# Optimization experiments

Hardware: AMD Instinct MI355X
Metric: run time of the kernel (lower is better)

## Reference

```python
import jax, jax.numpy as jnp
import numpy as np

N = 8192
IN_C = 256
OUT_C = 64
ALPHA = 0.2  # LeakyReLU negative slope
NEG_INF = -9e15


def setup_inputs() -> dict:
    key = jax.random.key(0)
    k1, k2, k3, k4 = jax.random.split(key, 4)
    x = jax.random.normal(k1, (N, IN_C), dtype=jnp.float32)
    adjacent = jax.random.randint(k2, (N, N), 0, 2, dtype=jnp.int32)
    # xavier_uniform with gain=1.2: limit = gain * sqrt(6/(fan_in+fan_out))
    lim_w = 1.2 * np.sqrt(6.0 / (IN_C + OUT_C))
    w = jax.random.uniform(k3, (IN_C, OUT_C), dtype=jnp.float32, minval=-lim_w, maxval=lim_w)
    lim_a = 1.2 * np.sqrt(6.0 / (2 * OUT_C + 1))
    a = jax.random.uniform(k4, (2 * OUT_C, 1), dtype=jnp.float32, minval=-lim_a, maxval=lim_a)
    return {"x": x, "adjacent": adjacent, "w": w, "a": a}


def reference(x, adjacent, w, a):
    # h: [N, out]
    h = x @ w
    # e_ij = LeakyReLU(a^T [h_i || h_j]) computed without materializing [N,N,2*out]:
    # split a into source/target halves -> rank-1 broadcast sum.
    a_src = a[:OUT_C, 0]   # [out]
    a_dst = a[OUT_C:, 0]   # [out]
    f_src = h @ a_src      # [N]
    f_dst = h @ a_dst      # [N]
    e = f_src[:, None] + f_dst[None, :]            # [N, N]
    e = jnp.where(e > 0, e, ALPHA * e)             # LeakyReLU
    # mask by adjacency, softmax over neighbors (rows)
    e = jnp.where(adjacent > 0, e, NEG_INF)
    attention = jax.nn.softmax(e, axis=-1)         # [N, N]
    h_prime = attention @ h                        # [N, out]
    # concat=True -> ELU activation
    return jax.nn.elu(h_prime)
```

## Files before the change

### kernel.cpp

```cpp
#include <hip/hip_runtime.h>
#include <hip/hip_bf16.h>

#define N 8192
#define IN_C 256
#define OUT_C 64
#define ALPHA 0.2f
#define L2E 1.44269504f

typedef short bf16x8 __attribute__((ext_vector_type(8)));
typedef float f32x4 __attribute__((ext_vector_type(4)));

#define OFF_H      0u
#define OFF_HT     2097152u
#define OFF_FS     3145728u
#define OFF_FD     3178496u
#define OFF_FDMAX  3211264u
#define OFF_NUM    3211520u

__global__ __launch_bounds__(256) void k_linear(const float* __restrict__ x,
                                                const float* __restrict__ w,
                                                const float* __restrict__ a,
                                                float* __restrict__ h,
                                                float* __restrict__ fs,
                                                float* __restrict__ fd) {
    __shared__ float wl[IN_C * OUT_C];
    int t = threadIdx.x;
    for (int idx = t; idx < IN_C * OUT_C; idx += 256) wl[idx] = w[idx];
    __syncthreads();
    int i = blockIdx.x * 4 + (t >> 6);
    int c = t & 63;
    const float* xr = x + (size_t)i * IN_C;
    float acc = 0.f;
#pragma unroll 8
    for (int k = 0; k < IN_C; ++k) acc = fmaf(xr[k], wl[k * 64 + c], acc);
    h[(size_t)i * 64 + c] = acc;
    float s = acc * a[c];
    float d = acc * a[64 + c];
#pragma unroll
    for (int off = 32; off > 0; off >>= 1) {
        s += __shfl_xor(s, off, 64);
        d += __shfl_xor(d, off, 64);
    }
    if (c == 0) { fs[i] = s; fd[i] = d; }
}

__global__ __launch_bounds__(256) void k_tr(const float* __restrict__ h,
                                            __hip_bfloat16* __restrict__ ht) {
    __shared__ __hip_bfloat16 lds[64 * 65];
    int t = threadIdx.x;
    int i0 = blockIdx.x * 64;
#pragma unroll
    for (int k = 0; k < 16; ++k) {
        int idx = k * 256 + t;
        int il = idx >> 6, c = idx & 63;
        lds[c * 65 + il] = __float2bfloat16(h[(size_t)(i0 + il) * 64 + c]);
    }
    __syncthreads();
#pragma unroll
    for (int k = 0; k < 16; ++k) {
        int idx = k * 256 + t;
        int c = idx >> 6, il = idx & 63;
        ht[(size_t)c * N + i0 + il] = lds[c * 65 + il];
    }
}

__global__ __launch_bounds__(256) void k_fdmax(const float* __restrict__ fd,
                                               float* __restrict__ out) {
    __shared__ float red[256];
    int t = threadIdx.x;
    float m = -3.4e38f;
    for (int j = t; j < N; j += 256) m = fmaxf(m, fd[j]);
    red[t] = m;
    __syncthreads();
    for (int s = 128; s > 0; s >>= 1) {
        if (t < s) red[t] = fmaxf(red[t], red[t + s]);
        __syncthreads();
    }
    if (t == 0) out[0] = red[0];
}

struct Stage {
    int4   ad0, ad1;
    float4 fd0, fd1;
    bf16x8 b0, b1, b2, b3;
};

__device__ __forceinline__ void load_stage(Stage& s,
        const int* __restrict__ arow, const float* __restrict__ fdst,
        const unsigned short* __restrict__ pb0, const unsigned short* __restrict__ pb1,
        const unsigned short* __restrict__ pb2, const unsigned short* __restrict__ pb3,
        int jb) {
    s.ad0 = *(const int4*)(arow + jb);
    s.ad1 = *(const int4*)(arow + jb + 4);
    s.fd0 = *(const float4*)(fdst + jb);
    s.fd1 = *(const float4*)(fdst + jb + 4);
    s.b0  = *(const bf16x8*)(pb0 + jb);
    s.b1  = *(const bf16x8*)(pb1 + jb);
    s.b2  = *(const bf16x8*)(pb2 + jb);
    s.b3  = *(const bf16x8*)(pb3 + jb);
}

__device__ __forceinline__ void compute_stage(const Stage& s, float fs, float mL,
        const bf16x8& bones,
        f32x4& acc0, f32x4& acc1, f32x4& acc2, f32x4& acc3, f32x4& acc4) {
    int   ad[8]  = {s.ad0.x, s.ad0.y, s.ad0.z, s.ad0.w, s.ad1.x, s.ad1.y, s.ad1.z, s.ad1.w};
    float fdv[8] = {s.fd0.x, s.fd0.y, s.fd0.z, s.fd0.w, s.fd1.x, s.fd1.y, s.fd1.z, s.fd1.w};
    bf16x8 af;
#pragma unroll
    for (int e = 0; e < 8; ++e) {
        float ee = fs + fdv[e];
        float l  = fmaxf(ee, ALPHA * ee);
        float a2 = __builtin_fmaf(l, L2E, -mL);
        float wt = __builtin_amdgcn_exp2f(a2);
        wt = (ad[e] > 0) ? wt : 0.f;
        __hip_bfloat16 hb = __float2bfloat16(wt);
        union { __hip_bfloat16 b; short s16; } u; u.b = hb;
        af[e] = u.s16;
    }
    acc0 = __builtin_amdgcn_mfma_f32_16x16x32_bf16(af, s.b0, acc0, 0, 0, 0);
    acc1 = __builtin_amdgcn_mfma_f32_16x16x32_bf16(af, s.b1, acc1, 0, 0, 0);
    acc2 = __builtin_amdgcn_mfma_f32_16x16x32_bf16(af, s.b2, acc2, 0, 0, 0);
    acc3 = __builtin_amdgcn_mfma_f32_16x16x32_bf16(af, s.b3, acc3, 0, 0, 0);
    acc4 = __builtin_amdgcn_mfma_f32_16x16x32_bf16(af, bones, acc4, 0, 0, 0);
}

__global__ __launch_bounds__(256, 4) void k_main(
    const int* __restrict__ adj,
    const float* __restrict__ fsrc,
    const float* __restrict__ fdst,
    const float* __restrict__ fdmax_p,
    const unsigned short* __restrict__ ht,
    float* __restrict__ nump,
    float* __restrict__ denp_out,
    int jch, int ns) {
    int bid = blockIdx.x;
    int rb = bid & 127;
    int kq = bid >> 7;
    int t = threadIdx.x;
    int wave = t >> 6;
    int lane = t & 63;
    int r  = lane & 15;
    int kg = lane >> 4;
    int i  = rb * 64 + wave * 16 + r;
    int j0 = kq * jch;

    float fs  = fsrc[i];
    float fdm = *fdmax_p;
    float e0  = fs + fdm;
    float m   = fmaxf(e0, ALPHA * e0);
    float mL  = m * L2E;

    const int* arow = adj + (size_t)i * N;
    const unsigned short* pb0 = ht + (size_t)(r)      * N;
    const unsigned short* pb1 = ht + (size_t)(16 + r) * N;
    const unsigned short* pb2 = ht + (size_t)(32 + r) * N;
    const unsigned short* pb3 = ht + (size_t)(48 + r) * N;

    bf16x8 bones;
#pragma unroll
    for (int e = 0; e < 8; ++e) bones[e] = (short)0x3F80;

    f32x4 acc0 = {0.f,0.f,0.f,0.f}, acc1 = {0.f,0.f,0.f,0.f};
    f32x4 acc2 = {0.f,0.f,0.f,0.f}, acc3 = {0.f,0.f,0.f,0.f};
    f32x4 acc4 = {0.f,0.f,0.f,0.f};

    int base = j0 + kg * 8;
    Stage A, B;
    load_stage(A, arow, fdst, pb0, pb1, pb2, pb3, base);
    load_stage(B, arow, fdst, pb0, pb1, pb2, pb3, base + 32);

#pragma unroll 1
    for (int ks = 0; ks < ns - 2; ks += 2) {
        compute_stage(A, fs, mL, bones, acc0, acc1, acc2, acc3, acc4);
        load_stage(A, arow, fdst, pb0, pb1, pb2, pb3, base + (ks + 2) * 32);
        compute_stage(B, fs, mL, bones, acc0, acc1, acc2, acc3, acc4);
        load_stage(B, arow, fdst, pb0, pb1, pb2, pb3, base + (ks + 3) * 32);
    }
    compute_stage(A, fs, mL, bones, acc0, acc1, acc2, acc3, acc4);
    compute_stage(B, fs, mL, bones, acc0, acc1, acc2, acc3, acc4);

    int orow = rb * 64 + wave * 16 + kg * 4;
    float* np = nump + (size_t)kq * N * 64;
#pragma unroll
    for (int rr = 0; rr < 4; ++rr) {
        np[(size_t)(orow + rr) * 64 + 0 * 16 + r] = acc0[rr];
        np[(size_t)(orow + rr) * 64 + 1 * 16 + r] = acc1[rr];
        np[(size_t)(orow + rr) * 64 + 2 * 16 + r] = acc2[rr];
        np[(size_t)(orow + rr) * 64 + 3 * 16 + r] = acc3[rr];
    }
    if (r == 0) {
#pragma unroll
        for (int rr = 0; rr < 4; ++rr) denp_out[kq * N + orow + rr] = acc4[rr];
    }
}

__global__ __launch_bounds__(256) void k_final(const float* __restrict__ nump,
                                               const float* __restrict__ denp,
                                               float* __restrict__ out,
                                               int kqn) {
    int gid = blockIdx.x * 256 + threadIdx.x;
    int base = gid * 4;
    int i = base >> 6;
    float4 num = {0.f, 0.f, 0.f, 0.f};
    float den = 0.f;
    for (int q = 0; q < kqn; ++q) {
        float4 v = *(const float4*)(nump + (size_t)q * (N * 64) + base);
        num.x += v.x; num.y += v.y; num.z += v.z; num.w += v.w;
        den += denp[q * N + i];
    }
    float rd = 1.f / den;
    float4 o;
    o.x = num.x * rd; o.y = num.y * rd; o.z = num.z * rd; o.w = num.w * rd;
    o.x = o.x > 0.f ? o.x : __expf(o.x) - 1.f;
    o.y = o.y > 0.f ? o.y : __expf(o.y) - 1.f;
    o.z = o.z > 0.f ? o.z : __expf(o.z) - 1.f;
    o.w = o.w > 0.f ? o.w : __expf(o.w) - 1.f;
    *(float4*)(out + base) = o;
}

extern "C" void kernel_launch(void* const* d_in, const int* in_sizes, int n_in,
                              void* d_out, int out_size, void* d_ws, size_t ws_size,
                              hipStream_t stream) {
    const float* x   = (const float*)d_in[0];
    const int*   adj = (const int*)d_in[1];
    const float* w   = (const float*)d_in[2];
    const float* a   = (const float*)d_in[3];
    float* out = (float*)d_out;
    char*  ws  = (char*)d_ws;

    float*          h    = (float*)(ws + OFF_H);
    __hip_bfloat16* ht   = (__hip_bfloat16*)(ws + OFF_HT);
    float*          fs   = (float*)(ws + OFF_FS);
    float*          fd   = (float*)(ws + OFF_FD);
    float*          fdm  = (float*)(ws + OFF_FDMAX);
    float*          nump = (float*)(ws + OFF_NUM);

    size_t need8 = (size_t)OFF_NUM + 8ull * N * 64 * 4 + 8ull * N * 4;
    int KQ = (ws_size >= need8) ? 8 : 4;
    float* denp = nump + (size_t)KQ * N * 64;
    int jch = N / KQ;
    int ns  = jch / 32;

    k_linear<<<2048, 256, 0, stream>>>(x, w, a, h, fs, fd);
    k_tr<<<128, 256, 0, stream>>>(h, ht);
    k_fdmax<<<1, 256, 0, stream>>>(fd, fdm);
    k_main<<<KQ * 128, 256, 0, stream>>>(adj, fs, fd, fdm,
                                         (const unsigned short*)ht, nump, denp, jch, ns);
    k_final<<<512, 256, 0, stream>>>(nump, denp, out, KQ);
}
```

Before: 468.7 us.

## Prepack adjacency tile into LDS bitmasks via wave ballots before MFMA loop

Each block now reads its whole adjacency slab up front with fully coalesced int4 loads, compresses it to 1-bit masks with __ballot, and stores them in shared memory. The main MFMA loop then pulls only fdst and the transposed h values from global memory and takes the mask bits from LDS. The aim is to replace the strided per-row int loads that were interleaved with compute by one coalesced streaming pass. The cost is a serial prologue per block with a barrier, no overlap between the adjacency read and compute, extra LDS use that may lower occupancy, and a final prefetch that wraps to index 0 instead of stopping.

```diff
diff --git a/kernel.cpp b/kernel.cpp
--- a/kernel.cpp
+++ b/kernel.cpp
@@ -9,6 +9,7 @@
 
 typedef short bf16x8 __attribute__((ext_vector_type(8)));
 typedef float f32x4 __attribute__((ext_vector_type(4)));
+typedef unsigned long long u64;
 
 #define OFF_H      0u
 #define OFF_HT     2097152u
@@ -79,19 +80,16 @@
     if (t == 0) out[0] = red[0];
 }
 
-struct Stage {
-    int4   ad0, ad1;
+struct HStage {
     float4 fd0, fd1;
     bf16x8 b0, b1, b2, b3;
 };
 
-__device__ __forceinline__ void load_stage(Stage& s,
-        const int* __restrict__ arow, const float* __restrict__ fdst,
+__device__ __forceinline__ void load_h(HStage& s,
+        const float* __restrict__ fdst,
         const unsigned short* __restrict__ pb0, const unsigned short* __restrict__ pb1,
         const unsigned short* __restrict__ pb2, const unsigned short* __restrict__ pb3,
         int jb) {
-    s.ad0 = *(const int4*)(arow + jb);
-    s.ad1 = *(const int4*)(arow + jb + 4);
     s.fd0 = *(const float4*)(fdst + jb);
     s.fd1 = *(const float4*)(fdst + jb + 4);
     s.b0  = *(const bf16x8*)(pb0 + jb);
@@ -100,19 +98,22 @@
     s.b3  = *(const bf16x8*)(pb3 + jb);
 }
 
-__device__ __forceinline__ void compute_stage(const Stage& s, float fs, float mL,
-        const bf16x8& bones,
+__device__ __forceinline__ void compute_h(const HStage& s,
+        u64 m0, u64 m1, u64 m2, u64 m3, int k8, int kg2,
+        float fs, float mL, const bf16x8& bones,
         f32x4& acc0, f32x4& acc1, f32x4& acc2, f32x4& acc3, f32x4& acc4) {
-    int   ad[8]  = {s.ad0.x, s.ad0.y, s.ad0.z, s.ad0.w, s.ad1.x, s.ad1.y, s.ad1.z, s.ad1.w};
     float fdv[8] = {s.fd0.x, s.fd0.y, s.fd0.z, s.fd0.w, s.fd1.x, s.fd1.y, s.fd1.z, s.fd1.w};
+    u64 msel[4] = {m0, m1, m2, m3};
     bf16x8 af;
 #pragma unroll
     for (int e = 0; e < 8; ++e) {
+        int sh = k8 * 8 + kg2 + (e >> 2);
+        unsigned bit = (unsigned)(msel[e & 3] >> sh) & 1u;
         float ee = fs + fdv[e];
         float l  = fmaxf(ee, ALPHA * ee);
         float a2 = __builtin_fmaf(l, L2E, -mL);
         float wt = __builtin_amdgcn_exp2f(a2);
-        wt = (ad[e] > 0) ? wt : 0.f;
+        wt = bit ? wt : 0.f;
         __hip_bfloat16 hb = __float2bfloat16(wt);
         union { __hip_bfloat16 b; short s16; } u; u.b = hb;
         af[e] = u.s16;
@@ -132,17 +133,38 @@
     const unsigned short* __restrict__ ht,
     float* __restrict__ nump,
     float* __restrict__ denp_out,
-    int jch, int ns) {
+    int jch, int ns, int groups) {
+    __shared__ u64 bits[64 * 34];
     int bid = blockIdx.x;
     int rb = bid & 127;
     int kq = bid >> 7;
     int t = threadIdx.x;
-    int wave = t >> 6;
-    int lane = t & 63;
-    int r  = lane & 15;
-    int kg = lane >> 4;
-    int i  = rb * 64 + wave * 16 + r;
+    int w = t >> 6;
+    int l = t & 63;
+    int r  = l & 15;
+    int kg = l >> 4;
+    int kg2 = kg * 2;
+    int ib0 = rb * 64;
+    int i  = ib0 + w * 16 + r;
     int j0 = kq * jch;
+    int strideU = groups * 4 + 2;
+
+    for (int rr2 = 0; rr2 < 16; ++rr2) {
+        int rowL = w * 16 + rr2;
+        const int* src = adj + (size_t)(ib0 + rowL) * N + j0;
+        for (int g = 0; g < groups; ++g) {
+            int4 v = *(const int4*)(src + g * 256 + l * 4);
+            u64 b0 = __ballot(v.x > 0);
+            u64 b1 = __ballot(v.y > 0);
+            u64 b2 = __ballot(v.z > 0);
+            u64 b3 = __ballot(v.w > 0);
+            if (l == 0) {
+                u64* p = &bits[rowL * strideU + g * 4];
+                p[0] = b0; p[1] = b1; p[2] = b2; p[3] = b3;
+            }
+        }
+    }
+    __syncthreads();
 
     float fs  = fsrc[i];
     float fdm = *fdmax_p;
@@ -150,7 +172,6 @@
     float m   = fmaxf(e0, ALPHA * e0);
     float mL  = m * L2E;
 
-    const int* arow = adj + (size_t)i * N;
     const unsigned short* pb0 = ht + (size_t)(r)      * N;
     const unsigned short* pb1 = ht + (size_t)(16 + r) * N;
     const unsigned short* pb2 = ht + (size_t)(32 + r) * N;
@@ -165,21 +186,32 @@
     f32x4 acc4 = {0.f,0.f,0.f,0.f};
 
     int base = j0 + kg * 8;
-    Stage A, B;
-    load_stage(A, arow, fdst, pb0, pb1, pb2, pb3, base);
-    load_stage(B, arow, fdst, pb0, pb1, pb2, pb3, base + 32);
+    int rowL = w * 16 + r;
+    HStage A, B;
+    load_h(A, fdst, pb0, pb1, pb2, pb3, base);
+    load_h(B, fdst, pb0, pb1, pb2, pb3, base + 32);
 
 #pragma unroll 1
-    for (int ks = 0; ks < ns - 2; ks += 2) {
-        compute_stage(A, fs, mL, bones, acc0, acc1, acc2, acc3, acc4);
-        load_stage(A, arow, fdst, pb0, pb1, pb2, pb3, base + (ks + 2) * 32);
-        compute_stage(B, fs, mL, bones, acc0, acc1, acc2, acc3, acc4);
-        load_stage(B, arow, fdst, pb0, pb1, pb2, pb3, base + (ks + 3) * 32);
-    }
-    compute_stage(A, fs, mL, bones, acc0, acc1, acc2, acc3, acc4);
-    compute_stage(B, fs, mL, bones, acc0, acc1, acc2, acc3, acc4);
-
-    int orow = rb * 64 + wave * 16 + kg * 4;
+    for (int g = 0; g < groups; ++g) {
+        const u64* mp = &bits[rowL * strideU + g * 4];
+        u64 m0 = mp[0], m1 = mp[1], m2 = mp[2], m3 = mp[3];
+#pragma unroll
+        for (int k8 = 0; k8 < 8; ++k8) {
+            int ks = g * 8 + k8;
+            int nxt = ks + 2 < ns ? ks + 2 : 0;
+            if (k8 & 1) {
+                compute_h(B, m0, m1, m2, m3, k8, kg2, fs, mL, bones,
+                          acc0, acc1, acc2, acc3, acc4);
+                load_h(B, fdst, pb0, pb1, pb2, pb3, base + nxt * 32);
+            } else {
+                compute_h(A, m0, m1, m2, m3, k8, kg2, fs, mL, bones,
+                          acc0, acc1, acc2, acc3, acc4);
+                load_h(A, fdst, pb0, pb1, pb2, pb3, base + nxt * 32);
+            }
+        }
+    }
+
+    int orow = ib0 + w * 16 + kg * 4;
     float* np = nump + (size_t)kq * N * 64;
 #pragma unroll
     for (int rr = 0; rr < 4; ++rr) {
@@ -240,11 +272,13 @@
     float* denp = nump + (size_t)KQ * N * 64;
     int jch = N / KQ;
     int ns  = jch / 32;
+    int groups = jch / 256;
 
     k_linear<<<2048, 256, 0, stream>>>(x, w, a, h, fs, fd);
     k_tr<<<128, 256, 0, stream>>>(h, ht);
     k_fdmax<<<1, 256, 0, stream>>>(fd, fdm);
     k_main<<<KQ * 128, 256, 0, stream>>>(adj, fs, fd, fdm,
-                                         (const unsigned short*)ht, nump, denp, jch, ns);
+                                         (const unsigned short*)ht, nump, denp,
+                                         jch, ns, groups);
     k_final<<<512, 256, 0, stream>>>(nump, denp, out, KQ);
 }
```

New measurement: 528.1 us. +12.7%, slower.
